# Performance work log

Hardware: AMD Instinct MI355X
Metric: run time of the kernel (lower is better)

## Reference

```python
import jax, jax.numpy as jnp
import numpy as np

B, S, D_MODEL = 2, 2048, 2048
N_HEADS, D_HEAD = 32, 64
SEQ_MAX = 2048


def _rope_cache(seq_len, d_head):
    half = d_head // 2
    inv_freq = 1.0 / (10000.0 ** (np.arange(0, half, dtype=np.float32) / half))
    t = np.arange(seq_len, dtype=np.float32)
    freqs = np.einsum('i,j->ij', t, inv_freq)  # [S, half]
    emb = np.concatenate([freqs, freqs], axis=-1)  # [S, d_head]
    return jnp.asarray(np.cos(emb)), jnp.asarray(np.sin(emb))


def _rotate_half(x):
    half = x.shape[-1] // 2
    return jnp.concatenate([-x[..., half:], x[..., :half]], axis=-1)


def setup_inputs() -> dict:
    key = jax.random.key(0)
    ks = jax.random.split(key, 9)
    std = 0.02
    mk = lambda k: jax.random.normal(k, (D_MODEL, D_MODEL), jnp.float32) * std
    return {
        'x': jax.random.normal(ks[0], (B, S, D_MODEL), jnp.float32),
        'Wq': mk(ks[1]), 'bq': jnp.zeros((D_MODEL,), jnp.float32),
        'Wk': mk(ks[2]), 'bk': jnp.zeros((D_MODEL,), jnp.float32),
        'Wv': mk(ks[3]), 'bv': jnp.zeros((D_MODEL,), jnp.float32),
        'Wo': mk(ks[4]), 'bo': jnp.zeros((D_MODEL,), jnp.float32),
    }


def reference(x, Wq, bq, Wk, bk, Wv, bv, Wo, bo):
    Bsz, S_len, _ = x.shape
    # projections (torch Linear: y = x @ W^T + b)
    q = x @ Wq.T + bq
    k = x @ Wk.T + bk
    v = x @ Wv.T + bv
    # [B, H, S, Dh]
    to_heads = lambda t: t.reshape(Bsz, S_len, N_HEADS, D_HEAD).transpose(0, 2, 1, 3)
    q, k, v = to_heads(q), to_heads(k), to_heads(v)
    cos, sin = _rope_cache(S_len, D_HEAD)  # [S, Dh]
    cos = cos[None, None]
    sin = sin[None, None]
    q = q * cos + _rotate_half(q) * sin
    k = k * cos + _rotate_half(k) * sin
    scale = 1.0 / jnp.sqrt(jnp.float32(D_HEAD))
    att = jnp.einsum('bhqd,bhkd->bhqk', q, k) * scale
    causal = jnp.tril(jnp.ones((S_len, S_len), dtype=bool))
    att = jnp.where(causal[None, None], att, jnp.float32(-jnp.inf))
    att = jax.nn.softmax(att, axis=-1)
    # sigmoid-gated values (dropout = identity at inference)
    y = jnp.einsum('bhqk,bhkd->bhqd', att, jax.nn.sigmoid(v))
    y = y.transpose(0, 2, 1, 3).reshape(Bsz, S_len, D_MODEL)
    return y @ Wo.T + bo
```

## Files before the change

### kernel.cpp

```cpp
#include <hip/hip_runtime.h>

typedef unsigned short u16;
typedef float f32x4 __attribute__((ext_vector_type(4)));
typedef __bf16 bf16x8 __attribute__((ext_vector_type(8)));

#define S_LEN 2048
#define DM 2048
#define NHEAD 32
#define DHEAD 64

__device__ __forceinline__ u16 f2bf(float f) {
    __bf16 b = (__bf16)f;
    return __builtin_bit_cast(u16, b);
}
__device__ __forceinline__ float bf2f(u16 u) {
    return (float)__builtin_bit_cast(__bf16, u);
}
__device__ __forceinline__ void async16(const void* g, void* l) {
    __builtin_amdgcn_global_load_lds(
        (const __attribute__((address_space(1))) unsigned int*)g,
        (__attribute__((address_space(3))) unsigned int*)l, 16, 0, 0);
}

__global__ __launch_bounds__(256) void cast_kernel(const float* __restrict__ in,
                                                   u16* __restrict__ out, long long n) {
    long long i = ((long long)blockIdx.x * 256 + threadIdx.x) * 4;
    if (i + 3 < n) {
        float4 f = *(const float4*)(in + i);
        ushort4 v;
        v.x = f2bf(f.x); v.y = f2bf(f.y); v.z = f2bf(f.z); v.w = f2bf(f.w);
        *(ushort4*)(out + i) = v;
    }
}

__global__ __launch_bounds__(256) void rope_kernel(u16* __restrict__ T, float scale) {
    int idx = blockIdx.x * 256 + threadIdx.x;
    int j = idx & 31;
    int h = (idx >> 5) & 31;
    long long row = idx >> 10;
    int s = (int)(row & (S_LEN - 1));
    long long base = row * DM + h * DHEAD;
    float inv = __expf(-(float)j * (9.210340371976184f / 32.0f));
    float th = (float)s * inv;
    float c = cosf(th), sn = sinf(th);
    float x1 = bf2f(T[base + j]);
    float x2 = bf2f(T[base + 32 + j]);
    T[base + j] = f2bf((x1 * c - x2 * sn) * scale);
    T[base + 32 + j] = f2bf((x2 * c + x1 * sn) * scale);
}

__global__ __launch_bounds__(256) void vsigt_kernel(const u16* __restrict__ V,
                                                    u16* __restrict__ VT) {
    int st = blockIdx.x & 63;
    int h = blockIdx.x >> 6;
    __shared__ u16 T[64][72];
    int r = threadIdx.x >> 2, c0 = (threadIdx.x & 3) * 16;
    const u16* src = V + (long long)(st * 64 + r) * DM + h * 64 + c0;
#pragma unroll
    for (int half = 0; half < 2; ++half) {
        bf16x8 v = *(const bf16x8*)(src + half * 8);
#pragma unroll
        for (int j = 0; j < 8; ++j) {
            float vf = (float)v[j];
            T[c0 + half * 8 + j][r] = f2bf(1.f / (1.f + __expf(-vf)));
        }
    }
    __syncthreads();
    int d = threadIdx.x >> 2, s0 = (threadIdx.x & 3) * 16;
    int b = st >> 5;
    int sl = (st & 31) * 64;
    u16* dst = VT + ((long long)((b * NHEAD + h) * DHEAD + d)) * S_LEN + sl + s0;
#pragma unroll
    for (int q = 0; q < 4; ++q)
        *(ushort4*)(dst + q * 4) = *(const ushort4*)(&T[d][s0] + q * 4);
}

__global__ __launch_bounds__(256) void gemm_qkv(const u16* __restrict__ A,
                                                const u16* __restrict__ Bt,
                                                const float* __restrict__ bq,
                                                const float* __restrict__ bk,
                                                const float* __restrict__ bv,
                                                u16* __restrict__ Qo, u16* __restrict__ Ko,
                                                u16* __restrict__ Vo, int M, int K) {
    __shared__ __align__(16) u16 As[128 * 32];
    __shared__ __align__(16) u16 Bs[128 * 32];
    int tid = threadIdx.x;
    int w = tid >> 6, lane = tid & 63, quad = lane >> 4, l16 = lane & 15;
    int m0 = blockIdx.x * 128;
    int n0 = blockIdx.y * 128;
    int sel = n0 >> 11;
    int nloc = n0 & 2047;
    u16* out = sel == 0 ? Qo : (sel == 1 ? Ko : Vo);
    const float* bias = sel == 0 ? bq : (sel == 1 ? bk : bv);
    int wm = (w & 1) * 64, wn = (w >> 1) * 64;

    f32x4 acc[4][4] = {};
    const u16* ga = A + (long long)m0 * K;
    const u16* gb = Bt + (long long)n0 * K;

    for (int k0 = 0; k0 < K; k0 += 32) {
#pragma unroll
        for (int rr = 0; rr < 2; ++rr) {
            int c = tid + rr * 256;
            int row = c >> 2, kc = c & 3;
            async16(ga + (long long)row * K + k0 + kc * 8, (char*)As + c * 16);
            async16(gb + (long long)row * K + k0 + kc * 8, (char*)Bs + c * 16);
        }
        __syncthreads();
        bf16x8 af[4], bfv[4];
#pragma unroll
        for (int mt = 0; mt < 4; ++mt)
            af[mt] = *(const bf16x8*)(As + (wm + mt * 16 + l16) * 32 + quad * 8);
#pragma unroll
        for (int nt = 0; nt < 4; ++nt)
            bfv[nt] = *(const bf16x8*)(Bs + (wn + nt * 16 + l16) * 32 + quad * 8);
#pragma unroll
        for (int mt = 0; mt < 4; ++mt)
#pragma unroll
            for (int nt = 0; nt < 4; ++nt)
                acc[mt][nt] = __builtin_amdgcn_mfma_f32_16x16x32_bf16(af[mt], bfv[nt],
                                                                      acc[mt][nt], 0, 0, 0);
        __syncthreads();
    }

#pragma unroll
    for (int mt = 0; mt < 4; ++mt) {
#pragma unroll
        for (int nt = 0; nt < 4; ++nt) {
            int col = nloc + wn + nt * 16 + l16;
            float bvs = bias[col];
#pragma unroll
            for (int r = 0; r < 4; ++r) {
                int row = m0 + wm + mt * 16 + quad * 4 + r;
                out[(long long)row * 2048 + col] = f2bf(acc[mt][nt][r] + bvs);
            }
        }
    }
}

__global__ __launch_bounds__(256) void gemm_bt_f32(const u16* __restrict__ A,
                                                   const u16* __restrict__ Bt,
                                                   const float* __restrict__ bias,
                                                   float* __restrict__ Cout,
                                                   int M, int N, int K) {
    __shared__ __align__(16) u16 As[128 * 32];
    __shared__ __align__(16) u16 Bs[128 * 32];
    int tid = threadIdx.x;
    int w = tid >> 6, lane = tid & 63, quad = lane >> 4, l16 = lane & 15;
    int m0 = blockIdx.x * 128;
    int n0 = blockIdx.y * 128;
    int wm = (w & 1) * 64, wn = (w >> 1) * 64;

    f32x4 acc[4][4] = {};
    const u16* ga = A + (long long)m0 * K;
    const u16* gb = Bt + (long long)n0 * K;

    for (int k0 = 0; k0 < K; k0 += 32) {
#pragma unroll
        for (int rr = 0; rr < 2; ++rr) {
            int c = tid + rr * 256;
            int row = c >> 2, kc = c & 3;
            async16(ga + (long long)row * K + k0 + kc * 8, (char*)As + c * 16);
            async16(gb + (long long)row * K + k0 + kc * 8, (char*)Bs + c * 16);
        }
        __syncthreads();
        bf16x8 af[4], bfv[4];
#pragma unroll
        for (int mt = 0; mt < 4; ++mt)
            af[mt] = *(const bf16x8*)(As + (wm + mt * 16 + l16) * 32 + quad * 8);
#pragma unroll
        for (int nt = 0; nt < 4; ++nt)
            bfv[nt] = *(const bf16x8*)(Bs + (wn + nt * 16 + l16) * 32 + quad * 8);
#pragma unroll
        for (int mt = 0; mt < 4; ++mt)
#pragma unroll
            for (int nt = 0; nt < 4; ++nt)
                acc[mt][nt] = __builtin_amdgcn_mfma_f32_16x16x32_bf16(af[mt], bfv[nt],
                                                                      acc[mt][nt], 0, 0, 0);
        __syncthreads();
    }

#pragma unroll
    for (int mt = 0; mt < 4; ++mt) {
#pragma unroll
        for (int nt = 0; nt < 4; ++nt) {
            int col = n0 + wn + nt * 16 + l16;
            float bvs = bias[col];
#pragma unroll
            for (int r = 0; r < 4; ++r) {
                int row = m0 + wm + mt * 16 + quad * 4 + r;
                Cout[(long long)row * N + col] = acc[mt][nt][r] + bvs;
            }
        }
    }
}

__global__ __launch_bounds__(256) void flash_attn(const u16* __restrict__ Q,
                                                  const u16* __restrict__ K,
                                                  const u16* __restrict__ VT,
                                                  u16* __restrict__ Y) {
    int bid = blockIdx.x;
    int pi = bid & 15;
    int h = (bid >> 4) & 31;
    int b = bid >> 9;
    int tid = threadIdx.x;
    int w = tid >> 6, lane = tid & 63, quad = lane >> 4, l16 = lane & 15;

    __shared__ __align__(16) u16 Kl[64 * 64];
    __shared__ __align__(16) u16 Vl[64 * 64];
    __shared__ __align__(16) u16 Pl[4][16 * 72];

    const u16* kbase = K + ((long long)(b * S_LEN)) * DM + h * DHEAD;
    const u16* vbase = VT + ((long long)((b * NHEAD + h) * DHEAD)) * S_LEN;

#pragma unroll 1
    for (int rep = 0; rep < 2; ++rep) {
        int qt = rep ? 31 - pi : pi;
        int qrow = qt * 64 + w * 16 + l16;
        const u16* qp = Q + ((long long)(b * S_LEN + qrow)) * DM + h * DHEAD + quad * 8;
        bf16x8 aq0 = *(const bf16x8*)(qp);
        bf16x8 aq1 = *(const bf16x8*)(qp + 32);

        f32x4 o[4] = {};
        float m_r = -__builtin_inff(), l_r = 0.f;

        for (int kt = 0; kt <= qt; ++kt) {
            int k0 = kt * 64;
#pragma unroll
            for (int rr = 0; rr < 2; ++rr) {
                int c = tid + rr * 256;
                int row = c >> 3;
                int lc = (c & 7) ^ (row & 7);
                async16(kbase + (long long)(k0 + row) * DM + lc * 8, (char*)Kl + c * 16);
                async16(vbase + (long long)row * S_LEN + k0 + lc * 8, (char*)Vl + c * 16);
            }
            __syncthreads();

            f32x4 s[4];
#pragma unroll
            for (int nt = 0; nt < 4; ++nt) {
                int row = nt * 16 + l16;
                int sw0 = (quad ^ (row & 7)) * 8;
                int sw1 = ((quad + 4) ^ (row & 7)) * 8;
                bf16x8 ak0 = *(const bf16x8*)(Kl + row * 64 + sw0);
                bf16x8 ak1 = *(const bf16x8*)(Kl + row * 64 + sw1);
                f32x4 a = {};
                a = __builtin_amdgcn_mfma_f32_16x16x32_bf16(ak0, aq0, a, 0, 0, 0);
                a = __builtin_amdgcn_mfma_f32_16x16x32_bf16(ak1, aq1, a, 0, 0, 0);
                s[nt] = a;
            }
            if (kt == qt) {
                int qg = qt * 64 + w * 16 + l16;
#pragma unroll
                for (int nt = 0; nt < 4; ++nt) {
#pragma unroll
                    for (int r = 0; r < 4; ++r) {
                        int kc = k0 + nt * 16 + quad * 4 + r;
                        if (kc > qg) s[nt][r] = -__builtin_inff();
                    }
                }
            }
            float mx = s[0][0];
#pragma unroll
            for (int nt = 0; nt < 4; ++nt)
#pragma unroll
                for (int r = 0; r < 4; ++r) mx = fmaxf(mx, s[nt][r]);
            mx = fmaxf(mx, __shfl_xor(mx, 16, 64));
            mx = fmaxf(mx, __shfl_xor(mx, 32, 64));
            float mnew = fmaxf(m_r, mx);
            float alpha = __expf(m_r - mnew);
            m_r = mnew;
#pragma unroll
            for (int nt = 0; nt < 4; ++nt)
#pragma unroll
                for (int r = 0; r < 4; ++r) s[nt][r] = __expf(s[nt][r] - mnew);
            float sum = 0.f;
#pragma unroll
            for (int nt = 0; nt < 4; ++nt)
#pragma unroll
                for (int r = 0; r < 4; ++r) sum += s[nt][r];
            sum += __shfl_xor(sum, 16, 64);
            sum += __shfl_xor(sum, 32, 64);
            l_r = l_r * alpha + sum;

            float al[4];
#pragma unroll
            for (int r = 0; r < 4; ++r)
                al[r] = __shfl(alpha, (lane & 48) | (quad * 4 + r), 64);
#pragma unroll
            for (int dt = 0; dt < 4; ++dt)
#pragma unroll
                for (int r = 0; r < 4; ++r) o[dt][r] *= al[r];

            u16* pw = &Pl[w][0];
#pragma unroll
            for (int nt = 0; nt < 4; ++nt) {
                ushort4 pk;
                pk.x = f2bf(s[nt][0]); pk.y = f2bf(s[nt][1]);
                pk.z = f2bf(s[nt][2]); pk.w = f2bf(s[nt][3]);
                *(ushort4*)(pw + l16 * 72 + nt * 16 + quad * 4) = pk;
            }
            bf16x8 ap0 = *(const bf16x8*)(pw + l16 * 72 + quad * 8);
            bf16x8 ap1 = *(const bf16x8*)(pw + l16 * 72 + 32 + quad * 8);
#pragma unroll
            for (int dt = 0; dt < 4; ++dt) {
                int row = dt * 16 + l16;
                int sw0 = (quad ^ (row & 7)) * 8;
                int sw1 = ((quad + 4) ^ (row & 7)) * 8;
                bf16x8 bv0 = *(const bf16x8*)(Vl + row * 64 + sw0);
                bf16x8 bv1 = *(const bf16x8*)(Vl + row * 64 + sw1);
                o[dt] = __builtin_amdgcn_mfma_f32_16x16x32_bf16(ap0, bv0, o[dt], 0, 0, 0);
                o[dt] = __builtin_amdgcn_mfma_f32_16x16x32_bf16(ap1, bv1, o[dt], 0, 0, 0);
            }
            __syncthreads();
        }

        float li[4];
#pragma unroll
        for (int r = 0; r < 4; ++r)
            li[r] = __shfl(l_r, (lane & 48) | (quad * 4 + r), 64);
#pragma unroll
        for (int dt = 0; dt < 4; ++dt) {
#pragma unroll
            for (int r = 0; r < 4; ++r) {
                int qg = qt * 64 + w * 16 + quad * 4 + r;
                Y[((long long)(b * S_LEN + qg)) * DM + h * DHEAD + dt * 16 + l16] =
                    f2bf(o[dt][r] / li[r]);
            }
        }
    }
}

extern "C" void kernel_launch(void* const* d_in, const int* in_sizes, int n_in,
                              void* d_out, int out_size, void* d_ws, size_t ws_size,
                              hipStream_t stream) {
    const float* x  = (const float*)d_in[0];
    const float* Wq = (const float*)d_in[1];
    const float* bq = (const float*)d_in[2];
    const float* Wk = (const float*)d_in[3];
    const float* bk = (const float*)d_in[4];
    const float* Wv = (const float*)d_in[5];
    const float* bv = (const float*)d_in[6];
    const float* Wo = (const float*)d_in[7];
    const float* bo = (const float*)d_in[8];

    const long long M = 2LL * S_LEN;
    const long long NX = M * DM;
    const long long NW = (long long)DM * DM;

    char* ws = (char*)d_ws;
    u16* xb   = (u16*)(ws);
    u16* Wqkv = (u16*)(ws + 16 * 1024 * 1024);
    u16* Wob  = (u16*)(ws + 40 * 1024 * 1024);
    u16* Qb   = (u16*)(ws + 48 * 1024 * 1024);
    u16* Kb   = (u16*)(ws + 64 * 1024 * 1024);
    u16* Vb   = (u16*)(ws + 80 * 1024 * 1024);
    u16* Yb   = (u16*)(ws + 96 * 1024 * 1024);
    u16* VTb  = xb;

    cast_kernel<<<(int)(NX / 1024), 256, 0, stream>>>(x, xb, NX);
    cast_kernel<<<(int)(NW / 1024), 256, 0, stream>>>(Wq, Wqkv, NW);
    cast_kernel<<<(int)(NW / 1024), 256, 0, stream>>>(Wk, Wqkv + NW, NW);
    cast_kernel<<<(int)(NW / 1024), 256, 0, stream>>>(Wv, Wqkv + 2 * NW, NW);
    cast_kernel<<<(int)(NW / 1024), 256, 0, stream>>>(Wo, Wob, NW);

    dim3 gqkv(32, 48);
    gemm_qkv<<<gqkv, 256, 0, stream>>>(xb, Wqkv, bq, bk, bv, Qb, Kb, Vb, (int)M, DM);

    rope_kernel<<<16384, 256, 0, stream>>>(Qb, 0.125f);
    rope_kernel<<<16384, 256, 0, stream>>>(Kb, 1.0f);

    vsigt_kernel<<<2048, 256, 0, stream>>>(Vb, VTb);

    flash_attn<<<2 * NHEAD * 16, 256, 0, stream>>>(Qb, Kb, VTb, Yb);

    dim3 gg(32, 16);
    gemm_bt_f32<<<gg, 256, 0, stream>>>(Yb, Wob, bo, (float*)d_out, (int)M, DM, DM);
}
```

Baseline: 470.4 us.

## Fuse RoPE and sigmoid-transpose into QKV GEMM epilogue; register-prefetch K/V in attention

Folds the RoPE rotation (with Q scaling) and the sigmoid plus transpose of V into the QKV GEMM epilogue. This removes three separate elementwise kernels and their global memory round trips. The RoPE angles are computed by incremental sincos rotation, which can drift slightly in precision. In flash attention, K/V tiles are now prefetched through registers one iteration ahead instead of async LDS loads, the PV MFMA operands are swapped so alpha and the output need no shuffles, and Y is written with vector stores. Launch bounds add a minimum-occupancy hint.

```diff
diff --git a/kernel.cpp b/kernel.cpp
--- a/kernel.cpp
+++ b/kernel.cpp
@@ -33,55 +33,13 @@
     }
 }
 
-__global__ __launch_bounds__(256) void rope_kernel(u16* __restrict__ T, float scale) {
-    int idx = blockIdx.x * 256 + threadIdx.x;
-    int j = idx & 31;
-    int h = (idx >> 5) & 31;
-    long long row = idx >> 10;
-    int s = (int)(row & (S_LEN - 1));
-    long long base = row * DM + h * DHEAD;
-    float inv = __expf(-(float)j * (9.210340371976184f / 32.0f));
-    float th = (float)s * inv;
-    float c = cosf(th), sn = sinf(th);
-    float x1 = bf2f(T[base + j]);
-    float x2 = bf2f(T[base + 32 + j]);
-    T[base + j] = f2bf((x1 * c - x2 * sn) * scale);
-    T[base + 32 + j] = f2bf((x2 * c + x1 * sn) * scale);
-}
-
-__global__ __launch_bounds__(256) void vsigt_kernel(const u16* __restrict__ V,
-                                                    u16* __restrict__ VT) {
-    int st = blockIdx.x & 63;
-    int h = blockIdx.x >> 6;
-    __shared__ u16 T[64][72];
-    int r = threadIdx.x >> 2, c0 = (threadIdx.x & 3) * 16;
-    const u16* src = V + (long long)(st * 64 + r) * DM + h * 64 + c0;
-#pragma unroll
-    for (int half = 0; half < 2; ++half) {
-        bf16x8 v = *(const bf16x8*)(src + half * 8);
-#pragma unroll
-        for (int j = 0; j < 8; ++j) {
-            float vf = (float)v[j];
-            T[c0 + half * 8 + j][r] = f2bf(1.f / (1.f + __expf(-vf)));
-        }
-    }
-    __syncthreads();
-    int d = threadIdx.x >> 2, s0 = (threadIdx.x & 3) * 16;
-    int b = st >> 5;
-    int sl = (st & 31) * 64;
-    u16* dst = VT + ((long long)((b * NHEAD + h) * DHEAD + d)) * S_LEN + sl + s0;
-#pragma unroll
-    for (int q = 0; q < 4; ++q)
-        *(ushort4*)(dst + q * 4) = *(const ushort4*)(&T[d][s0] + q * 4);
-}
-
 __global__ __launch_bounds__(256) void gemm_qkv(const u16* __restrict__ A,
                                                 const u16* __restrict__ Bt,
                                                 const float* __restrict__ bq,
                                                 const float* __restrict__ bk,
                                                 const float* __restrict__ bv,
                                                 u16* __restrict__ Qo, u16* __restrict__ Ko,
-                                                u16* __restrict__ Vo, int M, int K) {
+                                                u16* __restrict__ VTo, int M, int K) {
     __shared__ __align__(16) u16 As[128 * 32];
     __shared__ __align__(16) u16 Bs[128 * 32];
     int tid = threadIdx.x;
@@ -90,8 +48,6 @@
     int n0 = blockIdx.y * 128;
     int sel = n0 >> 11;
     int nloc = n0 & 2047;
-    u16* out = sel == 0 ? Qo : (sel == 1 ? Ko : Vo);
-    const float* bias = sel == 0 ? bq : (sel == 1 ? bk : bv);
     int wm = (w & 1) * 64, wn = (w >> 1) * 64;
 
     f32x4 acc[4][4] = {};
@@ -123,16 +79,58 @@
         __syncthreads();
     }
 
-#pragma unroll
-    for (int mt = 0; mt < 4; ++mt) {
-#pragma unroll
-        for (int nt = 0; nt < 4; ++nt) {
-            int col = nloc + wn + nt * 16 + l16;
-            float bvs = bias[col];
-#pragma unroll
-            for (int r = 0; r < 4; ++r) {
-                int row = m0 + wm + mt * 16 + quad * 4 + r;
-                out[(long long)row * 2048 + col] = f2bf(acc[mt][nt][r] + bvs);
+    if (sel < 2) {
+        float scale = sel == 0 ? 0.125f : 1.0f;
+        u16* out = sel == 0 ? Qo : Ko;
+        const float* bias = sel == 0 ? bq : bk;
+#pragma unroll
+        for (int ntl = 0; ntl < 2; ++ntl) {
+            int col = nloc + wn + ntl * 16 + l16;
+            int j = (wn + ntl * 16 + l16) & 63;
+            float inv = __expf(-(float)j * 0.28782313662425575f);
+            float ci, si;
+            sincosf(inv, &si, &ci);
+            float b1 = bias[col], b2 = bias[col + 32];
+#pragma unroll
+            for (int mt = 0; mt < 4; ++mt) {
+                int rowb = m0 + wm + mt * 16 + quad * 4;
+                int s0 = rowb & (S_LEN - 1);
+                float sn, cs;
+                sincosf((float)s0 * inv, &sn, &cs);
+#pragma unroll
+                for (int r = 0; r < 4; ++r) {
+                    int row = rowb + r;
+                    float x1 = acc[mt][ntl][r] + b1;
+                    float x2 = acc[mt][ntl + 2][r] + b2;
+                    out[(long long)row * 2048 + col] = f2bf((x1 * cs - x2 * sn) * scale);
+                    out[(long long)row * 2048 + col + 32] = f2bf((x2 * cs + x1 * sn) * scale);
+                    float c2 = cs * ci - sn * si;
+                    float s2 = sn * ci + cs * si;
+                    cs = c2; sn = s2;
+                }
+            }
+        }
+    } else {
+#pragma unroll
+        for (int mt = 0; mt < 4; ++mt) {
+            int rowb = m0 + wm + mt * 16 + quad * 4;
+            int b = rowb >> 11;
+            int s0 = rowb & (S_LEN - 1);
+#pragma unroll
+            for (int nt = 0; nt < 4; ++nt) {
+                int col = nloc + wn + nt * 16 + l16;
+                int h = col >> 6, d = col & 63;
+                float bvs = bv[col];
+                ushort4 pk;
+                float v0 = acc[mt][nt][0] + bvs;
+                float v1 = acc[mt][nt][1] + bvs;
+                float v2 = acc[mt][nt][2] + bvs;
+                float v3 = acc[mt][nt][3] + bvs;
+                pk.x = f2bf(1.f / (1.f + __expf(-v0)));
+                pk.y = f2bf(1.f / (1.f + __expf(-v1)));
+                pk.z = f2bf(1.f / (1.f + __expf(-v2)));
+                pk.w = f2bf(1.f / (1.f + __expf(-v3)));
+                *(ushort4*)(VTo + ((long long)((b * NHEAD + h) * DHEAD + d)) * S_LEN + s0) = pk;
             }
         }
     }
@@ -195,10 +193,10 @@
     }
 }
 
-__global__ __launch_bounds__(256) void flash_attn(const u16* __restrict__ Q,
-                                                  const u16* __restrict__ K,
-                                                  const u16* __restrict__ VT,
-                                                  u16* __restrict__ Y) {
+__global__ __launch_bounds__(256, 4) void flash_attn(const u16* __restrict__ Q,
+                                                     const u16* __restrict__ K,
+                                                     const u16* __restrict__ VT,
+                                                     u16* __restrict__ Y) {
     int bid = blockIdx.x;
     int pi = bid & 15;
     int h = (bid >> 4) & 31;
@@ -212,6 +210,18 @@
 
     const u16* kbase = K + ((long long)(b * S_LEN)) * DM + h * DHEAD;
     const u16* vbase = VT + ((long long)((b * NHEAD + h) * DHEAD)) * S_LEN;
+
+    bf16x8 kpre[2], vpre[2];
+    int c0 = tid, c1 = tid + 256;
+    int row0 = c0 >> 3, lc0 = (c0 & 7) ^ (row0 & 7);
+    int row1 = c1 >> 3, lc1 = (c1 & 7) ^ (row1 & 7);
+
+    {
+        kpre[0] = *(const bf16x8*)(kbase + (long long)row0 * DM + lc0 * 8);
+        vpre[0] = *(const bf16x8*)(vbase + (long long)row0 * S_LEN + lc0 * 8);
+        kpre[1] = *(const bf16x8*)(kbase + (long long)row1 * DM + lc1 * 8);
+        vpre[1] = *(const bf16x8*)(vbase + (long long)row1 * S_LEN + lc1 * 8);
+    }
 
 #pragma unroll 1
     for (int rep = 0; rep < 2; ++rep) {
@@ -224,15 +234,20 @@
         f32x4 o[4] = {};
         float m_r = -__builtin_inff(), l_r = 0.f;
 
+#pragma unroll 1
         for (int kt = 0; kt <= qt; ++kt) {
             int k0 = kt * 64;
-#pragma unroll
-            for (int rr = 0; rr < 2; ++rr) {
-                int c = tid + rr * 256;
-                int row = c >> 3;
-                int lc = (c & 7) ^ (row & 7);
-                async16(kbase + (long long)(k0 + row) * DM + lc * 8, (char*)Kl + c * 16);
-                async16(vbase + (long long)row * S_LEN + k0 + lc * 8, (char*)Vl + c * 16);
+            __syncthreads();
+            *(bf16x8*)((char*)Kl + c0 * 16) = kpre[0];
+            *(bf16x8*)((char*)Vl + c0 * 16) = vpre[0];
+            *(bf16x8*)((char*)Kl + c1 * 16) = kpre[1];
+            *(bf16x8*)((char*)Vl + c1 * 16) = vpre[1];
+            {
+                int nk0 = (kt < qt ? kt + 1 : 0) * 64;
+                kpre[0] = *(const bf16x8*)(kbase + (long long)(nk0 + row0) * DM + lc0 * 8);
+                vpre[0] = *(const bf16x8*)(vbase + (long long)row0 * S_LEN + nk0 + lc0 * 8);
+                kpre[1] = *(const bf16x8*)(kbase + (long long)(nk0 + row1) * DM + lc1 * 8);
+                vpre[1] = *(const bf16x8*)(vbase + (long long)row1 * S_LEN + nk0 + lc1 * 8);
             }
             __syncthreads();
 
@@ -283,14 +298,10 @@
             sum += __shfl_xor(sum, 32, 64);
             l_r = l_r * alpha + sum;
 
-            float al[4];
-#pragma unroll
-            for (int r = 0; r < 4; ++r)
-                al[r] = __shfl(alpha, (lane & 48) | (quad * 4 + r), 64);
 #pragma unroll
             for (int dt = 0; dt < 4; ++dt)
 #pragma unroll
-                for (int r = 0; r < 4; ++r) o[dt][r] *= al[r];
+                for (int r = 0; r < 4; ++r) o[dt][r] *= alpha;
 
             u16* pw = &Pl[w][0];
 #pragma unroll
@@ -300,33 +311,30 @@
                 pk.z = f2bf(s[nt][2]); pk.w = f2bf(s[nt][3]);
                 *(ushort4*)(pw + l16 * 72 + nt * 16 + quad * 4) = pk;
             }
-            bf16x8 ap0 = *(const bf16x8*)(pw + l16 * 72 + quad * 8);
-            bf16x8 ap1 = *(const bf16x8*)(pw + l16 * 72 + 32 + quad * 8);
+            bf16x8 bp0 = *(const bf16x8*)(pw + l16 * 72 + quad * 8);
+            bf16x8 bp1 = *(const bf16x8*)(pw + l16 * 72 + 32 + quad * 8);
 #pragma unroll
             for (int dt = 0; dt < 4; ++dt) {
                 int row = dt * 16 + l16;
                 int sw0 = (quad ^ (row & 7)) * 8;
                 int sw1 = ((quad + 4) ^ (row & 7)) * 8;
-                bf16x8 bv0 = *(const bf16x8*)(Vl + row * 64 + sw0);
-                bf16x8 bv1 = *(const bf16x8*)(Vl + row * 64 + sw1);
-                o[dt] = __builtin_amdgcn_mfma_f32_16x16x32_bf16(ap0, bv0, o[dt], 0, 0, 0);
-                o[dt] = __builtin_amdgcn_mfma_f32_16x16x32_bf16(ap1, bv1, o[dt], 0, 0, 0);
-            }
-            __syncthreads();
-        }
-
-        float li[4];
-#pragma unroll
-        for (int r = 0; r < 4; ++r)
-            li[r] = __shfl(l_r, (lane & 48) | (quad * 4 + r), 64);
+                bf16x8 av0 = *(const bf16x8*)(Vl + row * 64 + sw0);
+                bf16x8 av1 = *(const bf16x8*)(Vl + row * 64 + sw1);
+                o[dt] = __builtin_amdgcn_mfma_f32_16x16x32_bf16(av0, bp0, o[dt], 0, 0, 0);
+                o[dt] = __builtin_amdgcn_mfma_f32_16x16x32_bf16(av1, bp1, o[dt], 0, 0, 0);
+            }
+        }
+
+        float inv_l = 1.f / l_r;
+        u16* yp = Y + ((long long)(b * S_LEN + qt * 64 + w * 16 + l16)) * DM + h * DHEAD;
 #pragma unroll
         for (int dt = 0; dt < 4; ++dt) {
-#pragma unroll
-            for (int r = 0; r < 4; ++r) {
-                int qg = qt * 64 + w * 16 + quad * 4 + r;
-                Y[((long long)(b * S_LEN + qg)) * DM + h * DHEAD + dt * 16 + l16] =
-                    f2bf(o[dt][r] / li[r]);
-            }
+            ushort4 yk;
+            yk.x = f2bf(o[dt][0] * inv_l);
+            yk.y = f2bf(o[dt][1] * inv_l);
+            yk.z = f2bf(o[dt][2] * inv_l);
+            yk.w = f2bf(o[dt][3] * inv_l);
+            *(ushort4*)(yp + dt * 16 + quad * 4) = yk;
         }
     }
 }
@@ -354,9 +362,8 @@
     u16* Wob  = (u16*)(ws + 40 * 1024 * 1024);
     u16* Qb   = (u16*)(ws + 48 * 1024 * 1024);
     u16* Kb   = (u16*)(ws + 64 * 1024 * 1024);
-    u16* Vb   = (u16*)(ws + 80 * 1024 * 1024);
+    u16* VTb  = (u16*)(ws + 80 * 1024 * 1024);
     u16* Yb   = (u16*)(ws + 96 * 1024 * 1024);
-    u16* VTb  = xb;
 
     cast_kernel<<<(int)(NX / 1024), 256, 0, stream>>>(x, xb, NX);
     cast_kernel<<<(int)(NW / 1024), 256, 0, stream>>>(Wq, Wqkv, NW);
@@ -365,12 +372,7 @@
     cast_kernel<<<(int)(NW / 1024), 256, 0, stream>>>(Wo, Wob, NW);
 
     dim3 gqkv(32, 48);
-    gemm_qkv<<<gqkv, 256, 0, stream>>>(xb, Wqkv, bq, bk, bv, Qb, Kb, Vb, (int)M, DM);
-
-    rope_kernel<<<16384, 256, 0, stream>>>(Qb, 0.125f);
-    rope_kernel<<<16384, 256, 0, stream>>>(Kb, 1.0f);
-
-    vsigt_kernel<<<2048, 256, 0, stream>>>(Vb, VTb);
+    gemm_qkv<<<gqkv, 256, 0, stream>>>(xb, Wqkv, bq, bk, bv, Qb, Kb, VTb, (int)M, DM);
 
     flash_attn<<<2 * NHEAD * 16, 256, 0, stream>>>(Qb, Kb, VTb, Yb);
 
```

Result: faster. 459.0 us (-2.4%).
